# Kernel optimization log

Measured on AMD Instinct MI355X. Metric: run time of the kernel, lower is better.

## Reference

```python
import jax, jax.numpy as jnp
import numpy as np

DIM = 2048
K_DIM = 2048
Q_HEADS = 16
KV_HEADS = 4
HEAD_DIM = DIM // Q_HEADS  # 128
KV_DIM = HEAD_DIM * KV_HEADS  # 512
MAX_LEN = 2048
ROPE_THETA = 10000.0
ROPE_FACTOR = 8.0


def _rope_cos_sin(seq_len):
    # Faithful to generate_sin_cos_pos_emb with is_causal=True
    d = HEAD_DIM
    seq_eff = max(seq_len, MAX_LEN)
    base_adj = (ROPE_FACTOR * seq_eff / MAX_LEN - (ROPE_FACTOR - 1.0)) ** (d / (d - 2))
    adjusted_base = ROPE_THETA * base_adj
    inv_freq = 1.0 / adjusted_base ** (np.arange(0, d, 2, dtype=np.float32) / d)
    pos = np.arange(seq_len, dtype=np.float32)  # causal: no centering
    freqs = pos[:, None] * inv_freq[None, :]            # [S, d/2]
    emb = np.concatenate([freqs, freqs], axis=-1)        # [S, d]
    return jnp.asarray(np.cos(emb), jnp.float32), jnp.asarray(np.sin(emb), jnp.float32)


def _rotate_half(x):
    x1, x2 = jnp.split(x, 2, axis=-1)
    return jnp.concatenate([-x2, x1], axis=-1)


def setup_inputs() -> dict:
    key = jax.random.key(0)
    ks = jax.random.split(key, 12)
    B, S = 1, 2048
    s_in = 1.0 / np.sqrt(DIM)
    s_k = 1.0 / np.sqrt(K_DIM)
    return {
        "query": jax.random.normal(ks[0], (B, S, DIM), jnp.float32),
        "key": jax.random.normal(ks[1], (B, S, K_DIM), jnp.float32),
        "value": jax.random.normal(ks[2], (B, S, K_DIM), jnp.float32),
        "Wq": jax.random.uniform(ks[3], (DIM, DIM), jnp.float32, -s_in, s_in),
        "bq": jax.random.uniform(ks[4], (DIM,), jnp.float32, -s_in, s_in),
        "Wk": jax.random.uniform(ks[5], (KV_DIM, K_DIM), jnp.float32, -s_k, s_k),
        "bk": jax.random.uniform(ks[6], (KV_DIM,), jnp.float32, -s_k, s_k),
        "Wv": jax.random.uniform(ks[7], (KV_DIM, K_DIM), jnp.float32, -s_k, s_k),
        "bv": jax.random.uniform(ks[8], (KV_DIM,), jnp.float32, -s_k, s_k),
        "Wo": jax.random.uniform(ks[9], (DIM, DIM), jnp.float32, -s_in, s_in),
        "bo": jax.random.uniform(ks[10], (DIM,), jnp.float32, -s_in, s_in),
    }


def reference(query, key, value, Wq, bq, Wk, bk, Wv, bv, Wo, bo):
    B, S, _ = query.shape
    scale = HEAD_DIM ** -0.5

    q = query @ Wq.T + bq                                   # [B,S,DIM]
    k = key @ Wk.T + bk                                     # [B,S,KV_DIM]
    v = value @ Wv.T + bv                                   # [B,S,KV_DIM]

    q = q.reshape(B, S, Q_HEADS, HEAD_DIM)
    k = k.reshape(B, S, KV_HEADS, HEAD_DIM)
    v = v.reshape(B, S, KV_HEADS, HEAD_DIM)

    cos, sin = _rope_cos_sin(S)                              # [S,D]
    cos = cos[None, :, None, :]
    sin = sin[None, :, None, :]
    q = q * cos + _rotate_half(q) * sin
    k = k * cos + _rotate_half(k) * sin

    # [B,H,S,D]
    q = q.transpose(0, 2, 1, 3)
    k = k.transpose(0, 2, 1, 3)
    v = v.transpose(0, 2, 1, 3)

    rep = Q_HEADS // KV_HEADS
    k = jnp.repeat(k, rep, axis=1)
    v = jnp.repeat(v, rep, axis=1)

    scores = jnp.einsum('bhqd,bhkd->bhqk', q, k) * scale
    causal = jnp.tril(jnp.ones((S, S), bool))
    scores = jnp.where(causal[None, None], scores, jnp.finfo(scores.dtype).min)
    attn = jax.nn.softmax(scores, axis=-1)
    out = jnp.einsum('bhqk,bhkd->bhqd', attn, v)             # [B,H,S,D]

    out = out.transpose(0, 2, 1, 3).reshape(B, S, DIM)
    return out @ Wo.T + bo
```

## Files before the change

### kernel.cpp

```cpp
#include <hip/hip_runtime.h>
#include <stdint.h>

typedef __attribute__((ext_vector_type(8))) short short8;
typedef __attribute__((ext_vector_type(4))) float f32x4;
typedef __attribute__((ext_vector_type(4))) unsigned short u16x4;
typedef unsigned short bf16_t;

__device__ __forceinline__ bf16_t f2bf(float f) {
  union { float f; uint32_t u; } x; x.f = f;
  uint32_t r = x.u + 0x7fffu + ((x.u >> 16) & 1u);
  return (bf16_t)(r >> 16);
}

__device__ __forceinline__ void ld_g2l_16(const bf16_t* g, bf16_t* l) {
  __builtin_amdgcn_global_load_lds(
      (const __attribute__((address_space(1))) void*)g,
      (__attribute__((address_space(3))) void*)l, 16, 0, 0);
}

__global__ void rope_tab(float* __restrict__ CS, float* __restrict__ SN) {
  int idx = blockIdx.x * 256 + threadIdx.x;
  int i = idx & 63, pos = idx >> 6;
  float ang = (float)pos * exp2f((float)i * -0.2076205059f);
  CS[idx] = cosf(ang);
  SN[idx] = sinf(ang);
}

__global__ void convert_all(const float* __restrict__ s0, const float* __restrict__ s1,
                            const float* __restrict__ s2, const float* __restrict__ s3,
                            const float* __restrict__ s4, const float* __restrict__ s5,
                            const float* __restrict__ s6,
                            bf16_t* __restrict__ d0, bf16_t* __restrict__ d1,
                            bf16_t* __restrict__ d2, bf16_t* __restrict__ d3,
                            bf16_t* __restrict__ d4, bf16_t* __restrict__ d5,
                            bf16_t* __restrict__ d6) {
  int i = blockIdx.x * 256 + threadIdx.x;
  const float* src; bf16_t* dst; int off;
  if (i < 5 * 1048576) {
    int t = i >> 20; off = i & 1048575;
    if (t == 0)      { src = s0; dst = d0; }
    else if (t == 1) { src = s1; dst = d1; }
    else if (t == 2) { src = s2; dst = d2; }
    else if (t == 3) { src = s3; dst = d3; }
    else             { src = s4; dst = d4; }
  } else {
    int j = i - 5 * 1048576;
    if (j < 262144) { src = s5; dst = d5; off = j; }
    else            { src = s6; dst = d6; off = j - 262144; }
  }
  f32x4 v = *(const f32x4*)(src + (size_t)off * 4);
  u16x4 o;
  o[0] = f2bf(v[0]); o[1] = f2bf(v[1]); o[2] = f2bf(v[2]); o[3] = f2bf(v[3]);
  *(u16x4*)(dst + (size_t)off * 4) = o;
}

template <int MODE>
__device__ __forceinline__ void gemm_core(
    bf16_t* __restrict__ As, bf16_t* __restrict__ Bs,
    const bf16_t* __restrict__ A, const bf16_t* __restrict__ Bm,
    const float* __restrict__ bias, void* __restrict__ Cout,
    int N, int K, int m0, int n0,
    const float* __restrict__ CS, const float* __restrict__ SN) {
  const int tid = threadIdx.x;
  const int lane = tid & 63, quad = lane >> 4, l16 = lane & 15;
  const int wv = tid >> 6;
  const int m_off = wv * 32;
  const int c0 = tid, c1 = tid + 256;
  const int r0 = c0 >> 2, col0 = (c0 & 3) * 8;
  const int r1 = c1 >> 2, col1 = (c1 & 3) * 8;

  f32x4 acc[2][8];
  const f32x4 zf = {0.f, 0.f, 0.f, 0.f};
#pragma unroll
  for (int mi = 0; mi < 2; ++mi)
#pragma unroll
    for (int ni = 0; ni < 8; ++ni) acc[mi][ni] = zf;

  const bf16_t* Ap0 = A + (size_t)(m0 + r0) * K + col0;
  const bf16_t* Ap1 = A + (size_t)(m0 + r1) * K + col1;
  const bf16_t* Bp0 = Bm + (size_t)(n0 + r0) * K + col0;
  const bf16_t* Bp1 = Bm + (size_t)(n0 + r1) * K + col1;
  bf16_t* lA0 = As + c0 * 8;  bf16_t* lA1 = As + c1 * 8;
  bf16_t* lB0 = Bs + c0 * 8;  bf16_t* lB1 = Bs + c1 * 8;

  for (int k0 = 0; k0 < K; k0 += 32) {
    ld_g2l_16(Ap0 + k0, lA0);
    ld_g2l_16(Ap1 + k0, lA1);
    ld_g2l_16(Bp0 + k0, lB0);
    ld_g2l_16(Bp1 + k0, lB1);
    __syncthreads();
    short8 af[2], bf[8];
#pragma unroll
    for (int mi = 0; mi < 2; ++mi)
      af[mi] = *(const short8*)(&As[(m_off + mi * 16 + l16) * 32 + quad * 8]);
#pragma unroll
    for (int ni = 0; ni < 8; ++ni)
      bf[ni] = *(const short8*)(&Bs[(ni * 16 + l16) * 32 + quad * 8]);
#pragma unroll
    for (int mi = 0; mi < 2; ++mi)
#pragma unroll
      for (int ni = 0; ni < 8; ++ni)
        acc[mi][ni] = __builtin_amdgcn_mfma_f32_16x16x32_bf16(
            af[mi], bf[ni], acc[mi][ni], 0, 0, 0);
    __syncthreads();
  }

  if (MODE == 0 || MODE == 2) {
#pragma unroll
    for (int mi = 0; mi < 2; ++mi)
#pragma unroll
      for (int ni = 0; ni < 8; ++ni) {
        int n = n0 + ni * 16 + l16;
        int mbase = m0 + m_off + mi * 16 + quad * 4;
        float bv = bias[n];
#pragma unroll
        for (int r = 0; r < 4; ++r) {
          float v = acc[mi][ni][r] + bv;
          int m = mbase + r;
          if (MODE == 0) ((float*)Cout)[(size_t)m * N + n] = v;
          else           ((bf16_t*)Cout)[(size_t)n * 2048 + m] = f2bf(v);
        }
      }
  } else {
    const float scale = (MODE == 3) ? 0.08838834764831845f : 1.0f;
    bf16_t* dst = (bf16_t*)Cout;
#pragma unroll
    for (int mi = 0; mi < 2; ++mi)
#pragma unroll
      for (int r = 0; r < 4; ++r) {
        int m = m0 + m_off + mi * 16 + quad * 4 + r;
#pragma unroll
        for (int ni = 0; ni < 4; ++ni) {
          int i = ni * 16 + l16;
          int n_lo = n0 + i;
          float v1 = acc[mi][ni][r] + bias[n_lo];
          float v2 = acc[mi][ni + 4][r] + bias[n_lo + 64];
          float c = CS[m * 64 + i];
          float s = SN[m * 64 + i];
          float o1 = (v1 * c - v2 * s) * scale;
          float o2 = (v2 * c + v1 * s) * scale;
          dst[(size_t)m * N + n_lo] = f2bf(o1);
          dst[(size_t)m * N + n_lo + 64] = f2bf(o2);
        }
      }
  }
}

__global__ __launch_bounds__(256) void gemm_qkv(
    const bf16_t* __restrict__ qb, const bf16_t* __restrict__ kb,
    const bf16_t* __restrict__ vb, const bf16_t* __restrict__ wqb,
    const bf16_t* __restrict__ wkb, const bf16_t* __restrict__ wvb,
    const float* __restrict__ bq, const float* __restrict__ bk,
    const float* __restrict__ bv, bf16_t* __restrict__ Qr,
    bf16_t* __restrict__ Kr, bf16_t* __restrict__ Vt,
    const float* __restrict__ CS, const float* __restrict__ SN) {
  __shared__ __align__(16) bf16_t As[128 * 32];
  __shared__ __align__(16) bf16_t Bs[128 * 32];
  int bx = blockIdx.x, m0 = blockIdx.y * 128;
  if (bx < 16)
    gemm_core<3>(As, Bs, qb, wqb, bq, Qr, 2048, 2048, m0, bx * 128, CS, SN);
  else if (bx < 20)
    gemm_core<4>(As, Bs, kb, wkb, bk, Kr, 512, 2048, m0, (bx - 16) * 128, CS, SN);
  else
    gemm_core<2>(As, Bs, vb, wvb, bv, Vt, 512, 2048, m0, (bx - 20) * 128, CS, SN);
}

__global__ __launch_bounds__(256) void gemm_o(
    const bf16_t* __restrict__ Ob, const bf16_t* __restrict__ wob,
    const float* __restrict__ bo, float* __restrict__ out) {
  __shared__ __align__(16) bf16_t As[128 * 32];
  __shared__ __align__(16) bf16_t Bs[128 * 32];
  gemm_core<0>(As, Bs, Ob, wob, bo, out, 2048, 2048,
               blockIdx.y * 128, blockIdx.x * 128, nullptr, nullptr);
}

__global__ __launch_bounds__(256, 2) void attn_fwd(
    const bf16_t* __restrict__ Qr, const bf16_t* __restrict__ Kr,
    const bf16_t* __restrict__ Vt, bf16_t* __restrict__ Oo) {
  const int h = blockIdx.y;
  const int bx = blockIdx.x;
  const int qt = (h < 8) ? (31 - bx) : bx;
  const int T = qt + 1;

  const int tid = threadIdx.x;
  const int wv = tid >> 6, lane = tid & 63, quad = lane >> 4, l16 = lane & 15;
  const int q_base = qt * 64 + wv * 16;
  const int hkv = h >> 2;
  const int qg = q_base + l16;
  const int swzE = (l16 & 7) << 3;

  __shared__ __align__(16) bf16_t Ks[2][64 * 128];
  __shared__ __align__(16) bf16_t Vs[2][128 * 64];

  short8 qf[4];
  {
    const bf16_t* qp = Qr + (size_t)qg * 2048 + h * 128 + quad * 8;
#pragma unroll
    for (int kc = 0; kc < 4; ++kc) qf[kc] = *(const short8*)(qp + kc * 32);
  }

  const f32x4 zf = {0.f, 0.f, 0.f, 0.f};
  f32x4 o[8];
#pragma unroll
  for (int di = 0; di < 8; ++di) o[di] = zf;
  float l_acc = 0.f;

  auto STAGE = [&](int buf, int t) {
    const int k0 = t * 64;
    bf16_t* KB = &Ks[buf][0];
    bf16_t* VB = &Vs[buf][0];
#pragma unroll
    for (int m = 0; m < 4; ++m) {
      int rK = wv * 16 + m * 4 + (lane >> 4);
      const bf16_t* gK = Kr + (size_t)(k0 + rK) * 512 + hkv * 128
                         + (((lane & 15) ^ ((4 * (m & 1)) | quad)) << 3);
      ld_g2l_16(gK, KB + rK * 128 + ((lane & 15) << 3));
      int rV = wv * 32 + m * 8 + (lane >> 3);
      const bf16_t* gV = Vt + (size_t)(hkv * 128 + rV) * 2048 + k0
                         + (((lane & 7) ^ ((lane >> 3) & 7)) << 3);
      ld_g2l_16(gV, VB + rV * 64 + ((lane & 7) << 3));
    }
  };

  STAGE(0, 0);
  __syncthreads();
  int buf = 0;

  for (int t = 0; t < T; ++t) {
    if (t + 1 < T) STAGE(buf ^ 1, t + 1);
    const bf16_t* KB = &Ks[buf][0];
    const bf16_t* VB = &Vs[buf][0];
    const int k0 = t * 64;

    f32x4 sacc[4];
#pragma unroll
    for (int sub = 0; sub < 4; ++sub) sacc[sub] = zf;
#pragma unroll
    for (int sub = 0; sub < 4; ++sub)
#pragma unroll
      for (int kc = 0; kc < 4; ++kc) {
        short8 kf = *(const short8*)(
            &KB[(sub * 16 + l16) * 128 + ((kc * 32 + quad * 8) ^ swzE)]);
        sacc[sub] = __builtin_amdgcn_mfma_f32_16x16x32_bf16(kf, qf[kc], sacc[sub], 0, 0, 0);
      }

    const bool diag = (k0 + 63 > q_base);
    uint32_t Dw[4][2];
#pragma unroll
    for (int sub = 0; sub < 4; ++sub) {
      float pv[4];
#pragma unroll
      for (int r = 0; r < 4; ++r) {
        float e = __expf(sacc[sub][r]);
        if (diag) {
          int kg = k0 + sub * 16 + quad * 4 + r;
          if (kg > qg) e = 0.f;
        }
        pv[r] = e;
        l_acc += e;
      }
      Dw[sub][0] = (uint32_t)f2bf(pv[0]) | ((uint32_t)f2bf(pv[1]) << 16);
      Dw[sub][1] = (uint32_t)f2bf(pv[2]) | ((uint32_t)f2bf(pv[3]) << 16);
    }

    const int aA = ((((quad * 2) & 3) << 4) + l16) << 2;
    const int aB = ((((quad * 2 + 1) & 3) << 4) + l16) << 2;
    const bool losel = quad < 2;
#define BPERM(a, x) ((uint32_t)__builtin_amdgcn_ds_bpermute((a), (int)(x)))
    union { uint32_t w[4]; short8 v; } U0, U1;
    {
      uint32_t t0, t1;
      t0 = BPERM(aA, Dw[0][0]); t1 = BPERM(aA, Dw[1][0]); U0.w[0] = losel ? t0 : t1;
      t0 = BPERM(aA, Dw[0][1]); t1 = BPERM(aA, Dw[1][1]); U0.w[1] = losel ? t0 : t1;
      t0 = BPERM(aB, Dw[0][0]); t1 = BPERM(aB, Dw[1][0]); U0.w[2] = losel ? t0 : t1;
      t0 = BPERM(aB, Dw[0][1]); t1 = BPERM(aB, Dw[1][1]); U0.w[3] = losel ? t0 : t1;
      t0 = BPERM(aA, Dw[2][0]); t1 = BPERM(aA, Dw[3][0]); U1.w[0] = losel ? t0 : t1;
      t0 = BPERM(aA, Dw[2][1]); t1 = BPERM(aA, Dw[3][1]); U1.w[1] = losel ? t0 : t1;
      t0 = BPERM(aB, Dw[2][0]); t1 = BPERM(aB, Dw[3][0]); U1.w[2] = losel ? t0 : t1;
      t0 = BPERM(aB, Dw[2][1]); t1 = BPERM(aB, Dw[3][1]); U1.w[3] = losel ? t0 : t1;
    }
#undef BPERM
    const short8 pf0 = U0.v, pf1 = U1.v;

#pragma unroll
    for (int di = 0; di < 8; ++di) {
      short8 vf0 = *(const short8*)(
          &VB[(di * 16 + l16) * 64 + ((quad * 8) ^ swzE)]);
      short8 vf1 = *(const short8*)(
          &VB[(di * 16 + l16) * 64 + ((quad * 8 + 32) ^ swzE)]);
      o[di] = __builtin_amdgcn_mfma_f32_16x16x32_bf16(pf0, vf0, o[di], 0, 0, 0);
      o[di] = __builtin_amdgcn_mfma_f32_16x16x32_bf16(pf1, vf1, o[di], 0, 0, 0);
    }

    __asm__ volatile("s_waitcnt vmcnt(0)" ::: "memory");
    __syncthreads();
    buf ^= 1;
  }

  float lf = l_acc;
  lf += __shfl_xor(lf, 16);
  lf += __shfl_xor(lf, 32);
  float linv[4];
#pragma unroll
  for (int r = 0; r < 4; ++r) linv[r] = 1.0f / __shfl(lf, quad * 4 + r, 64);
#pragma unroll
  for (int di = 0; di < 8; ++di)
#pragma unroll
    for (int r = 0; r < 4; ++r) {
      size_t row = q_base + quad * 4 + r;
      size_t col = h * 128 + di * 16 + l16;
      Oo[row * 2048 + col] = f2bf(o[di][r] * linv[r]);
    }
}

extern "C" void kernel_launch(void* const* d_in, const int* in_sizes, int n_in,
                              void* d_out, int out_size, void* d_ws, size_t ws_size,
                              hipStream_t stream) {
  (void)in_sizes; (void)n_in; (void)out_size; (void)ws_size;
  const float* query = (const float*)d_in[0];
  const float* key = (const float*)d_in[1];
  const float* value = (const float*)d_in[2];
  const float* Wq = (const float*)d_in[3];
  const float* bq = (const float*)d_in[4];
  const float* Wk = (const float*)d_in[5];
  const float* bk = (const float*)d_in[6];
  const float* Wv = (const float*)d_in[7];
  const float* bv = (const float*)d_in[8];
  const float* Wo = (const float*)d_in[9];
  const float* bo = (const float*)d_in[10];
  float* out = (float*)d_out;

  char* ws = (char*)d_ws;
  const size_t MB = 1024 * 1024;
  bf16_t* qb  = (bf16_t*)(ws + 0 * MB);
  bf16_t* kb  = (bf16_t*)(ws + 8 * MB);
  bf16_t* vb  = (bf16_t*)(ws + 16 * MB);
  bf16_t* wqb = (bf16_t*)(ws + 24 * MB);
  bf16_t* wkb = (bf16_t*)(ws + 32 * MB);
  bf16_t* wvb = (bf16_t*)(ws + 34 * MB);
  bf16_t* wob = (bf16_t*)(ws + 36 * MB);
  bf16_t* Qr  = (bf16_t*)(ws + 44 * MB);
  bf16_t* Kr  = (bf16_t*)(ws + 52 * MB);
  bf16_t* Vt  = (bf16_t*)(ws + 54 * MB);
  bf16_t* Ob  = (bf16_t*)(ws + 56 * MB);
  float*  CS  = (float*)(ws + 64 * MB);
  float*  SN  = (float*)(ws + 64 * MB + 512 * 1024);

  rope_tab<<<512, 256, 0, stream>>>(CS, SN);
  convert_all<<<22528, 256, 0, stream>>>(query, key, value, Wq, Wo, Wk, Wv,
                                         qb, kb, vb, wqb, wob, wkb, wvb);
  gemm_qkv<<<dim3(24, 16), 256, 0, stream>>>(qb, kb, vb, wqb, wkb, wvb,
                                             bq, bk, bv, Qr, Kr, Vt, CS, SN);
  attn_fwd<<<dim3(32, 16), 256, 0, stream>>>(Qr, Kr, Vt, Ob);
  gemm_o<<<dim3(16, 16), 256, 0, stream>>>(Ob, wob, bo, out);
}
```

Measured before the change: 289.2 us.

## Software-pipeline QK^T one tile ahead, split K/V staging, use exp2 and packed bf16 cvt

Restructures the attention loop so the QK^T MFMAs for tile t+1 are issued while the softmax and PV work for tile t runs, with K staged two tiles ahead and V one tile ahead in separate lambdas. It folds log2(e) into the Q scale so the kernel can use exp2f in place of __expf, and it replaces software bf16 rounding with the v_cvt_pk_bf16_f32 instruction. This is meant to hide MFMA latency and shorten the exp and conversion path. In exchange it keeps two score register sets live and adds a prologue with extra syncs.

```diff
diff --git a/kernel.cpp b/kernel.cpp
--- a/kernel.cpp
+++ b/kernel.cpp
@@ -122,7 +122,7 @@
         }
       }
   } else {
-    const float scale = (MODE == 3) ? 0.08838834764831845f : 1.0f;
+    const float scale = (MODE == 3) ? 0.12751744f : 1.0f;
     bf16_t* dst = (bf16_t*)Cout;
 #pragma unroll
     for (int mi = 0; mi < 2; ++mi)
@@ -205,16 +205,22 @@
   for (int di = 0; di < 8; ++di) o[di] = zf;
   float l_acc = 0.f;
 
-  auto STAGE = [&](int buf, int t) {
+  auto STAGE_K = [&](int buf, int t) {
     const int k0 = t * 64;
     bf16_t* KB = &Ks[buf][0];
-    bf16_t* VB = &Vs[buf][0];
 #pragma unroll
     for (int m = 0; m < 4; ++m) {
       int rK = wv * 16 + m * 4 + (lane >> 4);
       const bf16_t* gK = Kr + (size_t)(k0 + rK) * 512 + hkv * 128
                          + (((lane & 15) ^ ((4 * (m & 1)) | quad)) << 3);
       ld_g2l_16(gK, KB + rK * 128 + ((lane & 15) << 3));
+    }
+  };
+  auto STAGE_V = [&](int buf, int t) {
+    const int k0 = t * 64;
+    bf16_t* VB = &Vs[buf][0];
+#pragma unroll
+    for (int m = 0; m < 4; ++m) {
       int rV = wv * 32 + m * 8 + (lane >> 3);
       const bf16_t* gV = Vt + (size_t)(hkv * 128 + rV) * 2048 + k0
                          + (((lane & 7) ^ ((lane >> 3) & 7)) << 3);
@@ -222,45 +228,44 @@
     }
   };
 
-  STAGE(0, 0);
-  __syncthreads();
-  int buf = 0;
-
-  for (int t = 0; t < T; ++t) {
-    if (t + 1 < T) STAGE(buf ^ 1, t + 1);
+  auto QK = [&](int buf, f32x4 (&s)[4]) {
     const bf16_t* KB = &Ks[buf][0];
-    const bf16_t* VB = &Vs[buf][0];
-    const int k0 = t * 64;
-
-    f32x4 sacc[4];
-#pragma unroll
-    for (int sub = 0; sub < 4; ++sub) sacc[sub] = zf;
+#pragma unroll
+    for (int sub = 0; sub < 4; ++sub) s[sub] = zf;
 #pragma unroll
     for (int sub = 0; sub < 4; ++sub)
 #pragma unroll
       for (int kc = 0; kc < 4; ++kc) {
         short8 kf = *(const short8*)(
             &KB[(sub * 16 + l16) * 128 + ((kc * 32 + quad * 8) ^ swzE)]);
-        sacc[sub] = __builtin_amdgcn_mfma_f32_16x16x32_bf16(kf, qf[kc], sacc[sub], 0, 0, 0);
+        s[sub] = __builtin_amdgcn_mfma_f32_16x16x32_bf16(kf, qf[kc], s[sub], 0, 0, 0);
       }
-
-    const bool diag = (k0 + 63 > q_base);
+  };
+
+  auto ITER = [&](int t, f32x4 (&cur)[4], f32x4 (&nxt)[4]) {
+    const int p = t & 1;
+    if (t + 2 < T) STAGE_K(p, t + 2);
+    if (t + 1 < T) STAGE_V(p ^ 1, t + 1);
+    if (t + 1 < T) QK(p ^ 1, nxt);
+
+    const int k0 = t * 64;
+    const bool dg = (k0 + 63 > q_base);
     uint32_t Dw[4][2];
 #pragma unroll
     for (int sub = 0; sub < 4; ++sub) {
       float pv[4];
 #pragma unroll
       for (int r = 0; r < 4; ++r) {
-        float e = __expf(sacc[sub][r]);
-        if (diag) {
+        float e = exp2f(cur[sub][r]);
+        if (dg) {
           int kg = k0 + sub * 16 + quad * 4 + r;
           if (kg > qg) e = 0.f;
         }
         pv[r] = e;
         l_acc += e;
       }
-      Dw[sub][0] = (uint32_t)f2bf(pv[0]) | ((uint32_t)f2bf(pv[1]) << 16);
-      Dw[sub][1] = (uint32_t)f2bf(pv[2]) | ((uint32_t)f2bf(pv[3]) << 16);
+      asm("v_cvt_pk_bf16_f32 %0, %1, %2" : "=v"(Dw[sub][0]) : "v"(pv[0]), "v"(pv[1]));
+      asm("v_cvt_pk_bf16_f32 %0, %1, %2" : "=v"(Dw[sub][1]) : "v"(pv[2]), "v"(pv[3]));
     }
 
     const int aA = ((((quad * 2) & 3) << 4) + l16) << 2;
@@ -282,6 +287,7 @@
 #undef BPERM
     const short8 pf0 = U0.v, pf1 = U1.v;
 
+    const bf16_t* VB = &Vs[p][0];
 #pragma unroll
     for (int di = 0; di < 8; ++di) {
       short8 vf0 = *(const short8*)(
@@ -294,7 +300,22 @@
 
     __asm__ volatile("s_waitcnt vmcnt(0)" ::: "memory");
     __syncthreads();
-    buf ^= 1;
+  };
+
+  f32x4 saccA[4], saccB[4];
+  STAGE_K(0, 0);
+  STAGE_V(0, 0);
+  if (T > 1) STAGE_K(1, 1);
+  __syncthreads();
+  QK(0, saccA);
+  __syncthreads();
+
+  int t = 0;
+  for (;;) {
+    ITER(t, saccA, saccB);
+    if (++t >= T) break;
+    ITER(t, saccB, saccA);
+    if (++t >= T) break;
   }
 
   float lf = l_acc;
```

New measurement: 286.9 us. Within noise of the previous version (-0.8%).

## Load attention K/V tiles straight from global into registers, dropping LDS staging

Applied to the files above, without the earlier changes.

The attention kernel no longer double-buffers K and V tiles in shared memory. Each wave now loads its K and V fragments directly from global memory into registers every iteration, which removes the per-tile barriers and LDS traffic. Three smaller changes ride along: the softmax exponent switches to exp2 with log2(e) folded into the Q scale, bf16 packing uses a hardware packed-convert instruction, and the per-head alternating block order is replaced by a uniform reverse order. The cost is that every wave fetches K/V redundantly from global or L2 with no prefetch, register pressure goes up, and the work ordering across heads changes.

```diff
diff --git a/kernel.cpp b/kernel.cpp
--- a/kernel.cpp
+++ b/kernel.cpp
@@ -122,7 +122,7 @@
         }
       }
   } else {
-    const float scale = (MODE == 3) ? 0.08838834764831845f : 1.0f;
+    const float scale = (MODE == 3) ? 0.12751744f : 1.0f;
     bf16_t* dst = (bf16_t*)Cout;
 #pragma unroll
     for (int mi = 0; mi < 2; ++mi)
@@ -178,8 +178,7 @@
     const bf16_t* __restrict__ Qr, const bf16_t* __restrict__ Kr,
     const bf16_t* __restrict__ Vt, bf16_t* __restrict__ Oo) {
   const int h = blockIdx.y;
-  const int bx = blockIdx.x;
-  const int qt = (h < 8) ? (31 - bx) : bx;
+  const int qt = 31 - blockIdx.x;
   const int T = qt + 1;
 
   const int tid = threadIdx.x;
@@ -187,10 +186,6 @@
   const int q_base = qt * 64 + wv * 16;
   const int hkv = h >> 2;
   const int qg = q_base + l16;
-  const int swzE = (l16 & 7) << 3;
-
-  __shared__ __align__(16) bf16_t Ks[2][64 * 128];
-  __shared__ __align__(16) bf16_t Vs[2][128 * 64];
 
   short8 qf[4];
   {
@@ -199,38 +194,30 @@
     for (int kc = 0; kc < 4; ++kc) qf[kc] = *(const short8*)(qp + kc * 32);
   }
 
+  const bf16_t* Kb = Kr + (size_t)hkv * 128 + (size_t)l16 * 512 + quad * 8;
+  const bf16_t* Vb = Vt + ((size_t)hkv * 128 + l16) * 2048 + quad * 8;
+
   const f32x4 zf = {0.f, 0.f, 0.f, 0.f};
   f32x4 o[8];
 #pragma unroll
   for (int di = 0; di < 8; ++di) o[di] = zf;
   float l_acc = 0.f;
 
-  auto STAGE = [&](int buf, int t) {
+  for (int t = 0; t < T; ++t) {
     const int k0 = t * 64;
-    bf16_t* KB = &Ks[buf][0];
-    bf16_t* VB = &Vs[buf][0];
-#pragma unroll
-    for (int m = 0; m < 4; ++m) {
-      int rK = wv * 16 + m * 4 + (lane >> 4);
-      const bf16_t* gK = Kr + (size_t)(k0 + rK) * 512 + hkv * 128
-                         + (((lane & 15) ^ ((4 * (m & 1)) | quad)) << 3);
-      ld_g2l_16(gK, KB + rK * 128 + ((lane & 15) << 3));
-      int rV = wv * 32 + m * 8 + (lane >> 3);
-      const bf16_t* gV = Vt + (size_t)(hkv * 128 + rV) * 2048 + k0
-                         + (((lane & 7) ^ ((lane >> 3) & 7)) << 3);
-      ld_g2l_16(gV, VB + rV * 64 + ((lane & 7) << 3));
-    }
-  };
-
-  STAGE(0, 0);
-  __syncthreads();
-  int buf = 0;
-
-  for (int t = 0; t < T; ++t) {
-    if (t + 1 < T) STAGE(buf ^ 1, t + 1);
-    const bf16_t* KB = &Ks[buf][0];
-    const bf16_t* VB = &Vs[buf][0];
-    const int k0 = t * 64;
+
+    short8 kf[4][4];
+#pragma unroll
+    for (int sub = 0; sub < 4; ++sub)
+#pragma unroll
+      for (int kc = 0; kc < 4; ++kc)
+        kf[sub][kc] = *(const short8*)(Kb + (size_t)(k0 + sub * 16) * 512 + kc * 32);
+    short8 vf[8][2];
+#pragma unroll
+    for (int di = 0; di < 8; ++di) {
+      vf[di][0] = *(const short8*)(Vb + (size_t)(di * 16) * 2048 + k0);
+      vf[di][1] = *(const short8*)(Vb + (size_t)(di * 16) * 2048 + k0 + 32);
+    }
 
     f32x4 sacc[4];
 #pragma unroll
@@ -238,29 +225,27 @@
 #pragma unroll
     for (int sub = 0; sub < 4; ++sub)
 #pragma unroll
-      for (int kc = 0; kc < 4; ++kc) {
-        short8 kf = *(const short8*)(
-            &KB[(sub * 16 + l16) * 128 + ((kc * 32 + quad * 8) ^ swzE)]);
-        sacc[sub] = __builtin_amdgcn_mfma_f32_16x16x32_bf16(kf, qf[kc], sacc[sub], 0, 0, 0);
-      }
-
-    const bool diag = (k0 + 63 > q_base);
+      for (int kc = 0; kc < 4; ++kc)
+        sacc[sub] = __builtin_amdgcn_mfma_f32_16x16x32_bf16(
+            kf[sub][kc], qf[kc], sacc[sub], 0, 0, 0);
+
+    const bool dg = (k0 + 63 > q_base);
     uint32_t Dw[4][2];
 #pragma unroll
     for (int sub = 0; sub < 4; ++sub) {
       float pv[4];
 #pragma unroll
       for (int r = 0; r < 4; ++r) {
-        float e = __expf(sacc[sub][r]);
-        if (diag) {
+        float e = exp2f(sacc[sub][r]);
+        if (dg) {
           int kg = k0 + sub * 16 + quad * 4 + r;
           if (kg > qg) e = 0.f;
         }
         pv[r] = e;
         l_acc += e;
       }
-      Dw[sub][0] = (uint32_t)f2bf(pv[0]) | ((uint32_t)f2bf(pv[1]) << 16);
-      Dw[sub][1] = (uint32_t)f2bf(pv[2]) | ((uint32_t)f2bf(pv[3]) << 16);
+      asm("v_cvt_pk_bf16_f32 %0, %1, %2" : "=v"(Dw[sub][0]) : "v"(pv[0]), "v"(pv[1]));
+      asm("v_cvt_pk_bf16_f32 %0, %1, %2" : "=v"(Dw[sub][1]) : "v"(pv[2]), "v"(pv[3]));
     }
 
     const int aA = ((((quad * 2) & 3) << 4) + l16) << 2;
@@ -284,17 +269,9 @@
 
 #pragma unroll
     for (int di = 0; di < 8; ++di) {
-      short8 vf0 = *(const short8*)(
-          &VB[(di * 16 + l16) * 64 + ((quad * 8) ^ swzE)]);
-      short8 vf1 = *(const short8*)(
-          &VB[(di * 16 + l16) * 64 + ((quad * 8 + 32) ^ swzE)]);
-      o[di] = __builtin_amdgcn_mfma_f32_16x16x32_bf16(pf0, vf0, o[di], 0, 0, 0);
-      o[di] = __builtin_amdgcn_mfma_f32_16x16x32_bf16(pf1, vf1, o[di], 0, 0, 0);
-    }
-
-    __asm__ volatile("s_waitcnt vmcnt(0)" ::: "memory");
-    __syncthreads();
-    buf ^= 1;
+      o[di] = __builtin_amdgcn_mfma_f32_16x16x32_bf16(pf0, vf[di][0], o[di], 0, 0, 0);
+      o[di] = __builtin_amdgcn_mfma_f32_16x16x32_bf16(pf1, vf[di][1], o[di], 0, 0, 0);
+    }
   }
 
   float lf = l_acc;
```

Result: slower. 458.5 us (+58.6%).

## Shrink GEMM tiles to 64x128 with 2x2 wave layout; use exp2 and packed bf16 convert

Applied to the files above, without the earlier changes.

The projection GEMMs move from 128x128 tiles to 64x128 tiles with a 2x2 wave arrangement, doubling the grid so more blocks fill the CUs. Each block does less work and has less register pressure, at the cost of more redundant B-tile loads. Attention switches to exp2f with log2(e) folded into the Q scale, and uses the hardware packed bf16 convert instead of manual rounding.

```diff
diff --git a/kernel.cpp b/kernel.cpp
--- a/kernel.cpp
+++ b/kernel.cpp
@@ -64,42 +64,40 @@
   const int tid = threadIdx.x;
   const int lane = tid & 63, quad = lane >> 4, l16 = lane & 15;
   const int wv = tid >> 6;
-  const int m_off = wv * 32;
-  const int c0 = tid, c1 = tid + 256;
-  const int r0 = c0 >> 2, col0 = (c0 & 3) * 8;
-  const int r1 = c1 >> 2, col1 = (c1 & 3) * 8;
-
-  f32x4 acc[2][8];
+  const int wr = wv >> 1, wc = wv & 1;
+
+  f32x4 acc[2][4];
   const f32x4 zf = {0.f, 0.f, 0.f, 0.f};
 #pragma unroll
   for (int mi = 0; mi < 2; ++mi)
 #pragma unroll
-    for (int ni = 0; ni < 8; ++ni) acc[mi][ni] = zf;
-
-  const bf16_t* Ap0 = A + (size_t)(m0 + r0) * K + col0;
-  const bf16_t* Ap1 = A + (size_t)(m0 + r1) * K + col1;
-  const bf16_t* Bp0 = Bm + (size_t)(n0 + r0) * K + col0;
-  const bf16_t* Bp1 = Bm + (size_t)(n0 + r1) * K + col1;
-  bf16_t* lA0 = As + c0 * 8;  bf16_t* lA1 = As + c1 * 8;
-  bf16_t* lB0 = Bs + c0 * 8;  bf16_t* lB1 = Bs + c1 * 8;
+    for (int ni = 0; ni < 4; ++ni) acc[mi][ni] = zf;
+
+  const int rA = tid >> 2, cA = (tid & 3) * 8;
+  const bf16_t* Ap  = A + (size_t)(m0 + rA) * K + cA;
+  const bf16_t* Bp0 = Bm + (size_t)(n0 + rA) * K + cA;
+  const bf16_t* Bp1 = Bm + (size_t)(n0 + 64 + rA) * K + cA;
+  bf16_t* lA  = As + tid * 8;
+  bf16_t* lB0 = Bs + tid * 8;
+  bf16_t* lB1 = Bs + (tid + 256) * 8;
 
   for (int k0 = 0; k0 < K; k0 += 32) {
-    ld_g2l_16(Ap0 + k0, lA0);
-    ld_g2l_16(Ap1 + k0, lA1);
+    ld_g2l_16(Ap + k0, lA);
     ld_g2l_16(Bp0 + k0, lB0);
     ld_g2l_16(Bp1 + k0, lB1);
     __syncthreads();
-    short8 af[2], bf[8];
+    short8 af[2], bf[4];
 #pragma unroll
     for (int mi = 0; mi < 2; ++mi)
-      af[mi] = *(const short8*)(&As[(m_off + mi * 16 + l16) * 32 + quad * 8]);
-#pragma unroll
-    for (int ni = 0; ni < 8; ++ni)
-      bf[ni] = *(const short8*)(&Bs[(ni * 16 + l16) * 32 + quad * 8]);
+      af[mi] = *(const short8*)(&As[(wr * 32 + mi * 16 + l16) * 32 + quad * 8]);
+#pragma unroll
+    for (int ni = 0; ni < 4; ++ni)
+      bf[ni] = *(const short8*)(
+          &Bs[(wc * 32 + (ni & 1) * 16 + (ni >> 1) * 64 + l16) * 32 + quad * 8]);
 #pragma unroll
     for (int mi = 0; mi < 2; ++mi)
 #pragma unroll
-      for (int ni = 0; ni < 8; ++ni)
+      for (int ni = 0; ni < 4; ++ni)
         acc[mi][ni] = __builtin_amdgcn_mfma_f32_16x16x32_bf16(
             af[mi], bf[ni], acc[mi][ni], 0, 0, 0);
     __syncthreads();
@@ -109,9 +107,9 @@
 #pragma unroll
     for (int mi = 0; mi < 2; ++mi)
 #pragma unroll
-      for (int ni = 0; ni < 8; ++ni) {
-        int n = n0 + ni * 16 + l16;
-        int mbase = m0 + m_off + mi * 16 + quad * 4;
+      for (int ni = 0; ni < 4; ++ni) {
+        int n = n0 + wc * 32 + (ni & 1) * 16 + (ni >> 1) * 64 + l16;
+        int mbase = m0 + wr * 32 + mi * 16 + quad * 4;
         float bv = bias[n];
 #pragma unroll
         for (int r = 0; r < 4; ++r) {
@@ -122,19 +120,19 @@
         }
       }
   } else {
-    const float scale = (MODE == 3) ? 0.08838834764831845f : 1.0f;
+    const float scale = (MODE == 3) ? 0.12751744f : 1.0f;
     bf16_t* dst = (bf16_t*)Cout;
 #pragma unroll
     for (int mi = 0; mi < 2; ++mi)
 #pragma unroll
       for (int r = 0; r < 4; ++r) {
-        int m = m0 + m_off + mi * 16 + quad * 4 + r;
-#pragma unroll
-        for (int ni = 0; ni < 4; ++ni) {
-          int i = ni * 16 + l16;
+        int m = m0 + wr * 32 + mi * 16 + quad * 4 + r;
+#pragma unroll
+        for (int ni = 0; ni < 2; ++ni) {
+          int i = wc * 32 + ni * 16 + l16;
           int n_lo = n0 + i;
           float v1 = acc[mi][ni][r] + bias[n_lo];
-          float v2 = acc[mi][ni + 4][r] + bias[n_lo + 64];
+          float v2 = acc[mi][ni + 2][r] + bias[n_lo + 64];
           float c = CS[m * 64 + i];
           float s = SN[m * 64 + i];
           float o1 = (v1 * c - v2 * s) * scale;
@@ -154,9 +152,9 @@
     const float* __restrict__ bv, bf16_t* __restrict__ Qr,
     bf16_t* __restrict__ Kr, bf16_t* __restrict__ Vt,
     const float* __restrict__ CS, const float* __restrict__ SN) {
-  __shared__ __align__(16) bf16_t As[128 * 32];
+  __shared__ __align__(16) bf16_t As[64 * 32];
   __shared__ __align__(16) bf16_t Bs[128 * 32];
-  int bx = blockIdx.x, m0 = blockIdx.y * 128;
+  int bx = blockIdx.x, m0 = blockIdx.y * 64;
   if (bx < 16)
     gemm_core<3>(As, Bs, qb, wqb, bq, Qr, 2048, 2048, m0, bx * 128, CS, SN);
   else if (bx < 20)
@@ -168,10 +166,10 @@
 __global__ __launch_bounds__(256) void gemm_o(
     const bf16_t* __restrict__ Ob, const bf16_t* __restrict__ wob,
     const float* __restrict__ bo, float* __restrict__ out) {
-  __shared__ __align__(16) bf16_t As[128 * 32];
+  __shared__ __align__(16) bf16_t As[64 * 32];
   __shared__ __align__(16) bf16_t Bs[128 * 32];
   gemm_core<0>(As, Bs, Ob, wob, bo, out, 2048, 2048,
-               blockIdx.y * 128, blockIdx.x * 128, nullptr, nullptr);
+               blockIdx.y * 64, blockIdx.x * 128, nullptr, nullptr);
 }
 
 __global__ __launch_bounds__(256, 2) void attn_fwd(
@@ -244,23 +242,23 @@
         sacc[sub] = __builtin_amdgcn_mfma_f32_16x16x32_bf16(kf, qf[kc], sacc[sub], 0, 0, 0);
       }
 
-    const bool diag = (k0 + 63 > q_base);
+    const bool dg = (k0 + 63 > q_base);
     uint32_t Dw[4][2];
 #pragma unroll
     for (int sub = 0; sub < 4; ++sub) {
       float pv[4];
 #pragma unroll
       for (int r = 0; r < 4; ++r) {
-        float e = __expf(sacc[sub][r]);
-        if (diag) {
+        float e = exp2f(sacc[sub][r]);
+        if (dg) {
           int kg = k0 + sub * 16 + quad * 4 + r;
           if (kg > qg) e = 0.f;
         }
         pv[r] = e;
         l_acc += e;
       }
-      Dw[sub][0] = (uint32_t)f2bf(pv[0]) | ((uint32_t)f2bf(pv[1]) << 16);
-      Dw[sub][1] = (uint32_t)f2bf(pv[2]) | ((uint32_t)f2bf(pv[3]) << 16);
+      asm("v_cvt_pk_bf16_f32 %0, %1, %2" : "=v"(Dw[sub][0]) : "v"(pv[0]), "v"(pv[1]));
+      asm("v_cvt_pk_bf16_f32 %0, %1, %2" : "=v"(Dw[sub][1]) : "v"(pv[2]), "v"(pv[3]));
     }
 
     const int aA = ((((quad * 2) & 3) << 4) + l16) << 2;
@@ -349,8 +347,8 @@
   rope_tab<<<512, 256, 0, stream>>>(CS, SN);
   convert_all<<<22528, 256, 0, stream>>>(query, key, value, Wq, Wo, Wk, Wv,
                                          qb, kb, vb, wqb, wob, wkb, wvb);
-  gemm_qkv<<<dim3(24, 16), 256, 0, stream>>>(qb, kb, vb, wqb, wkb, wvb,
+  gemm_qkv<<<dim3(24, 32), 256, 0, stream>>>(qb, kb, vb, wqb, wkb, wvb,
                                              bq, bk, bv, Qr, Kr, Vt, CS, SN);
   attn_fwd<<<dim3(32, 16), 256, 0, stream>>>(Qr, Kr, Vt, Ob);
-  gemm_o<<<dim3(16, 16), 256, 0, stream>>>(Ob, wob, bo, out);
-}
+  gemm_o<<<dim3(16, 32), 256, 0, stream>>>(Ob, wob, bo, out);
+}
```

New measurement: 273.5 us. 5.4% less time.
